# Optimization experiments

Measured on AMD Instinct MI355X. Metric: run time of the kernel, lower is better.

The kernel has to match this reference:

```python
import jax, jax.numpy as jnp
import numpy as np
import math

H = 12  # num_heads
LOGIT_SCALE_MAX = math.log(1.0 / 0.01)  # ~4.60517


def setup_inputs() -> dict:
    key = jax.random.key(0)
    ks = jax.random.split(key, 4)
    L, N, C = 1024, 8, 768
    scale = (C // H) ** -0.5
    return {
        "x": jax.random.normal(ks[0], (L, N, C), jnp.float32),
        "in_proj_weight": jax.random.normal(ks[1], (3 * C, C), jnp.float32) * scale,
        "in_proj_bias": jnp.zeros((3 * C,), jnp.float32),
        "logit_scale": jnp.full((H, 1, 1), jnp.log(10.0), jnp.float32),
        "head_scale": jnp.ones((H, 1, 1), jnp.float32),
        "out_w": jax.random.normal(ks[2], (C, C), jnp.float32) * scale,
        "out_b": jnp.zeros((C,), jnp.float32),
    }


def _normalize(t, eps=1e-12):
    # torch F.normalize: x / max(||x||, eps)
    n = jnp.linalg.norm(t, axis=-1, keepdims=True)
    return t / jnp.maximum(n, eps)


def reference(x, in_proj_weight, in_proj_bias, logit_scale, head_scale, out_w, out_b):
    L, N, C = x.shape
    D = C // H
    qkv = x @ in_proj_weight.T + in_proj_bias  # (L, N, 3C)
    q, k, v = jnp.split(qkv, 3, axis=-1)

    def to_heads(t):  # (L, N, C) -> (N, H, L, D); matches view(L, N*H, D).transpose(0,1)
        return t.reshape(L, N, H, D).transpose(1, 2, 0, 3)

    q, k, v = to_heads(q), to_heads(k), to_heads(v)
    # scaled-cosine attention: cosine sim * clamped-exp learnable logit scale
    attn = jnp.einsum('nhld,nhmd->nhlm', _normalize(q), _normalize(k))  # (N,H,L,L)
    ls = jnp.exp(jnp.minimum(logit_scale, LOGIT_SCALE_MAX))  # (H,1,1)
    attn = attn * ls[None]
    attn = jax.nn.softmax(attn, axis=-1)
    o = jnp.einsum('nhlm,nhmd->nhld', attn, v)  # (N,H,L,D)
    o = o * head_scale[None]  # per-head scale
    o = o.transpose(2, 0, 1, 3).reshape(L, N, C)  # back to (L, N, C)
    return o @ out_w.T + out_b
```

## Files before the change

### kernel.cpp

```cpp
#include <hip/hip_runtime.h>
#include <stdint.h>
#include <math.h>

typedef unsigned short u16;
typedef _Float16 f16;
typedef __attribute__((ext_vector_type(4))) float f32x4;
typedef __attribute__((ext_vector_type(8))) f16 h8;
typedef __attribute__((ext_vector_type(4))) f16 h4;
typedef __attribute__((ext_vector_type(2))) f16 h2;
typedef __attribute__((ext_vector_type(2))) __fp16 fp16x2;
typedef __attribute__((ext_vector_type(2))) unsigned int u32x2;
typedef __attribute__((ext_vector_type(4))) unsigned int u32x4;
typedef __attribute__((ext_vector_type(4))) unsigned short u16x4;
typedef __attribute__((ext_vector_type(8))) unsigned short u16x8;

typedef const __attribute__((address_space(1))) u16 gas_u16;
typedef __attribute__((address_space(3))) u16 las_u16;

#define MFMA32(a,b,c) __builtin_amdgcn_mfma_f32_16x16x32_f16((a),(b),(c),0,0,0)
#define MFMA16(a,b,c) __builtin_amdgcn_mfma_f32_16x16x16f16((a),(b),(c),0,0,0)

__device__ __forceinline__ float h2f(u16 h){ f16 x; __builtin_memcpy(&x,&h,2); return (float)x; }
__device__ __forceinline__ u16 f2h(float f){ f16 x = (f16)f; u16 u; __builtin_memcpy(&u,&x,2); return u; }

__device__ __forceinline__ float fast_exp2(float x){
#if __has_builtin(__builtin_amdgcn_exp2f)
  return __builtin_amdgcn_exp2f(x);
#else
  return exp2f(x);
#endif
}

__device__ __forceinline__ h2 pkrtz(float a, float b){
  fp16x2 t = __builtin_amdgcn_cvt_pkrtz(a, b);
  h2 r; __builtin_memcpy(&r, &t, 4);
  return r;
}

#define NA4 1572864
#define NB4 442368
#define NC4 147456
__global__ __launch_bounds__(256) void cvt3_kernel(
    const float* __restrict__ a, u16* __restrict__ da,
    const float* __restrict__ b, u16* __restrict__ db,
    const float* __restrict__ c, u16* __restrict__ dc)
{
  int i = blockIdx.x*256 + threadIdx.x;
  const float* s; u16* d; int off;
  if (i < NA4)            { s = a; d = da; off = i; }
  else if (i < NA4+NB4)   { s = b; d = db; off = i - NA4; }
  else if (i < NA4+NB4+NC4){ s = c; d = dc; off = i - NA4 - NB4; }
  else return;
  f32x4 v = ((const f32x4*)s)[off];
  u16x4 o;
  o[0]=f2h(v[0]); o[1]=f2h(v[1]); o[2]=f2h(v[2]); o[3]=f2h(v[3]);
  ((u16x4*)d)[off] = o;
}

__global__ __launch_bounds__(256) void gemm_kernel(
    const u16* __restrict__ A, const u16* __restrict__ B, const float* __restrict__ bias,
    int mode, u16* __restrict__ qh, u16* __restrict__ kh, u16* __restrict__ vtp,
    float* __restrict__ outp, const float* __restrict__ lsb)
{
  __shared__ u16 lA[2][128*64];
  __shared__ u16 lB[2][128*64];
  const int tid = threadIdx.x;
  const int lane = tid & 63;
  const int w = tid >> 6, wr = w >> 1, wc = w & 1;
  const int lo = lane & 15, hi = lane >> 4;

  const int bx = blockIdx.x, by = blockIdx.y;

  f32x4 zero = {0.f,0.f,0.f,0.f};
  f32x4 acc[4][4];
#pragma unroll
  for (int a=0;a<4;a++)
#pragma unroll
    for (int b=0;b<4;b++) acc[a][b] = zero;
  const u16* Ag = A + (size_t)bx*128*768;
  const u16* Bg = B + (size_t)by*128*768;
  const int srow = tid >> 3;
  const int scol = (((tid & 7) ^ (srow & 7)) * 8);

#define STAGE(buf, kt) do { \
    _Pragma("unroll") \
    for (int j=0;j<4;j++) { \
      __builtin_amdgcn_global_load_lds((gas_u16*)(Ag + (size_t)(j*32+srow)*768 + (kt) + scol), (las_u16*)(&lA[buf][j*2048 + tid*8]), 16, 0, 0); \
      __builtin_amdgcn_global_load_lds((gas_u16*)(Bg + (size_t)(j*32+srow)*768 + (kt) + scol), (las_u16*)(&lB[buf][j*2048 + tid*8]), 16, 0, 0); \
    } \
  } while(0)

  STAGE(0, 0);
#pragma unroll
  for (int t = 0; t < 12; ++t) {
    const int cur = t & 1;
    if (t < 11) {
      STAGE(cur^1, (t+1)*64);
      asm volatile("s_waitcnt vmcnt(8)" ::: "memory");
    } else {
      asm volatile("s_waitcnt vmcnt(0)" ::: "memory");
    }
    __builtin_amdgcn_sched_barrier(0);
    __builtin_amdgcn_s_barrier();
#pragma unroll
    for (int s=0;s<2;s++) {
      const int kk = s ^ (w & 1);
      h8 af[4], bfr[4];
#pragma unroll
      for (int mf=0; mf<4; mf++) {
        int r = wr*64 + mf*16 + lo;
        af[mf]  = *(const h8*)(&lA[cur][r*64 + (((hi + 4*kk) ^ (lo & 7)) * 8)]);
      }
#pragma unroll
      for (int nf=0; nf<4; nf++) {
        int r = wc*64 + nf*16 + lo;
        bfr[nf] = *(const h8*)(&lB[cur][r*64 + (((hi + 4*kk) ^ (lo & 7)) * 8)]);
      }
#pragma unroll
      for (int mf=0; mf<4; mf++)
#pragma unroll
        for (int nf=0; nf<4; nf++)
          acc[mf][nf] = MFMA32(af[mf], bfr[nf], acc[mf][nf]);
    }
    asm volatile("s_waitcnt lgkmcnt(0)" ::: "memory");
    __builtin_amdgcn_sched_barrier(0);
    __builtin_amdgcn_s_barrier();
  }
#undef STAGE

  const int r0 = bx*128 + wr*64;
  const int j0 = by*128 + wc*64;
  if (mode == 0) {
    const int p = (j0 >= 1536) ? 2 : ((j0 >= 768) ? 1 : 0);
    float bi[4];
#pragma unroll
    for (int nf=0;nf<4;nf++) bi[nf] = bias[j0 + nf*16 + lo];
    if (p == 2) {
      u16* Tt = (wc == 0) ? (u16*)lA : (u16*)lB;
      const int cbase = wr*16;
#pragma unroll
      for (int mf=0; mf<4; mf++)
#pragma unroll
        for (int nf=0; nf<4; nf++) {
          int d = nf*16 + lo;
          int c = cbase + mf*4 + hi;
          u16x4 pk;
#pragma unroll
          for (int i=0;i<4;i++) pk[i] = f2h(acc[mf][nf][i] + bi[nf]);
          *(u16x4*)(Tt + d*128 + ((c ^ ((d & 7) << 2)) << 2)) = pk;
        }
      __syncthreads();
      const int hh0 = 2*by - 24;
#pragma unroll
      for (int kq=0; kq<8; kq++) {
        int idx = tid + kq*256;
        int nn  = idx & 7;
        int d   = (idx >> 3) & 63;
        int lh  = (idx >> 9) & 1;
        int wcc = idx >> 10;
        const u16* Ts = (wcc == 0) ? (const u16*)lA : (const u16*)lB;
        u16x8 v8;
#pragma unroll
        for (int ll=0; ll<8; ll++) {
          int rl = (lh*8 + ll)*8 + nn;
          int c  = rl >> 2;
          v8[ll] = Ts[d*128 + ((c ^ ((d & 7) << 2)) << 2) + (rl & 3)];
        }
        size_t off = (((size_t)nn*12 + hh0 + wcc)*64 + d)*1024 + (size_t)bx*16 + lh*8;
        *(u16x8*)(vtp + off) = v8;
      }
    } else {
      const int c0 = j0 - p*768;
      const int hh = c0 >> 6;
      u16* dst = (p==0) ? qh : kh;
      float qsc = 1.0f;
      if (p == 0) qsc = __expf(fminf(lsb[hh], 4.6051701859880913680f)) * 1.4426950408889634f;
#pragma unroll
      for (int mf=0; mf<4; mf++)
#pragma unroll
        for (int i=0;i<4;i++) {
          int r = r0 + mf*16 + 4*hi + i;
          int n = r & 7, l = r >> 3;
          float v[4]; float ss = 0.f;
#pragma unroll
          for (int nf=0;nf<4;nf++){ v[nf] = acc[mf][nf][i] + bi[nf]; ss += v[nf]*v[nf]; }
          ss += __shfl_xor(ss, 1);
          ss += __shfl_xor(ss, 2);
          ss += __shfl_xor(ss, 4);
          ss += __shfl_xor(ss, 8);
          float sc = qsc / fmaxf(sqrtf(ss), 1e-12f);
          size_t base = (((size_t)n*12 + hh)*1024 + l)*64;
#pragma unroll
          for (int nf=0;nf<4;nf++)
            dst[base + nf*16 + lo] = f2h(v[nf]*sc);
        }
    }
  } else {
#pragma unroll
    for (int nf=0; nf<4; nf++) {
      int j = j0 + nf*16 + lo;
      float bi = bias[j];
#pragma unroll
      for (int mf=0; mf<4; mf++)
#pragma unroll
        for (int i=0;i<4;i++) {
          int r = r0 + mf*16 + 4*hi + i;
          outp[(size_t)r*768 + j] = acc[mf][nf][i] + bi;
        }
    }
  }
}

__global__ __launch_bounds__(256, 3) void flash_kernel(
    const u16* __restrict__ qh, const u16* __restrict__ kh, const u16* __restrict__ vt,
    u16* __restrict__ obuf, const float* __restrict__ hsv, const float* __restrict__ lsp)
{
  __shared__ u16 lK[2][64*64];
  __shared__ u16 lVT[2][64*64];
  const int lin = blockIdx.y*8 + blockIdx.x;
  const int xcd = lin & 7, g = lin >> 3;
  const int nh = xcd + 8*(g >> 3);
  const int qt = g & 7;
  const int h = nh % 12, n = nh / 12;
  const u16* Qp = qh + (size_t)nh*65536;
  const u16* Kp = kh + (size_t)nh*65536;
  const u16* Vp = vt + (size_t)nh*65536;
  const int tid = threadIdx.x, lane = tid & 63, w = tid >> 6;
  const int lo = lane & 15, hi = lane >> 4;
  const int e = lo & 7;

  h8 qa0, qa1, qb0, qb1;
  {
    const u16* qrow = Qp + (size_t)(qt*128 + w*32 + lo)*64 + hi*8;
    qa0 = *(const h8*)qrow;          qa1 = *(const h8*)(qrow + 32);
    qb0 = *(const h8*)(qrow + 1024); qb1 = *(const h8*)(qrow + 1024 + 32);
  }
  const f32x4 zero = {0.f,0.f,0.f,0.f};
  f32x4 oA[4] = {zero,zero,zero,zero};
  f32x4 oB[4] = {zero,zero,zero,zero};
  f32x4 lA4 = zero, lB4 = zero;
  const h4 ones = {(f16)1.f,(f16)1.f,(f16)1.f,(f16)1.f};

  float OFF;
  {
    float b = __expf(fminf(lsp[h], 4.6051701859880913680f)) * 1.4426950408889634f;
    OFF = fmaxf(b - 15.5f, 0.f);
  }

  const int sr = tid >> 2;
  const int c4 = tid & 3;
  const int sx1 = sr & 7;
  const int sx2 = (sr & 7) << 1;

  u32x4 ka, kb, va, vb;
  ka = *(const u32x4*)(Kp + (size_t)sr*64 + c4*16);
  kb = *(const u32x4*)(Kp + (size_t)sr*64 + c4*16 + 8);
  va = *(const u32x4*)(Vp + (size_t)sr*1024 + c4*16);
  vb = *(const u32x4*)(Vp + (size_t)sr*1024 + c4*16 + 8);

#define STAGE_WRITE(bf) do { \
    u16* kr = lK[bf] + sr*64; \
    *(u32x4*)(kr + (((2*c4)   ^ sx1) << 3)) = ka; \
    *(u32x4*)(kr + (((2*c4+1) ^ sx1) << 3)) = kb; \
    u16* vr = lVT[bf] + sr*64; \
    *(u32x2*)(vr + (((( 0|c4) ^ sx2) << 2))) = (u32x2){va[0], va[1]}; \
    *(u32x2*)(vr + (((( 4|c4) ^ sx2) << 2))) = (u32x2){va[2], va[3]}; \
    *(u32x2*)(vr + (((( 8|c4) ^ sx2) << 2))) = (u32x2){vb[0], vb[1]}; \
    *(u32x2*)(vr + ((((12|c4) ^ sx2) << 2))) = (u32x2){vb[2], vb[3]}; \
  } while(0)

  STAGE_WRITE(0);
  asm volatile("s_waitcnt lgkmcnt(0)" ::: "memory");
  __builtin_amdgcn_sched_barrier(0);
  __builtin_amdgcn_s_barrier();

  for (int t = 0; t < 16; ++t) {
    const int cb = t & 1;
    if (t < 15) {
      ka = *(const u32x4*)(Kp + (size_t)(t+1)*4096 + (size_t)sr*64 + c4*16);
      kb = *(const u32x4*)(Kp + (size_t)(t+1)*4096 + (size_t)sr*64 + c4*16 + 8);
      va = *(const u32x4*)(Vp + (size_t)sr*1024 + (t+1)*64 + c4*16);
      vb = *(const u32x4*)(Vp + (size_t)sr*1024 + (t+1)*64 + c4*16 + 8);
    }
    f32x4 sa[4], sb[4];
#pragma unroll
    for (int kf=0; kf<4; kf++) {
      const u16* krow = lK[cb] + (kf*16 + lo)*64;
      h8 k0 = *(const h8*)(krow + (((hi  ) ^ e) << 3));
      h8 k1 = *(const h8*)(krow + (((hi+4) ^ e) << 3));
      sa[kf] = MFMA32(k1, qa1, MFMA32(k0, qa0, zero));
      sb[kf] = MFMA32(k1, qb1, MFMA32(k0, qb0, zero));
    }
    if (OFF != 0.f) {
#pragma unroll
      for (int kf=0;kf<4;kf++)
#pragma unroll
        for (int i=0;i<4;i++) { sa[kf][i] -= OFF; sb[kf][i] -= OFF; }
    }
    h4 pa[4], pb[4];
#pragma unroll
    for (int kf=0;kf<4;kf++) {
      h2 a01 = pkrtz(fast_exp2(sa[kf][0]), fast_exp2(sa[kf][1]));
      h2 a23 = pkrtz(fast_exp2(sa[kf][2]), fast_exp2(sa[kf][3]));
      pa[kf] = __builtin_shufflevector(a01, a23, 0, 1, 2, 3);
      h2 b01 = pkrtz(fast_exp2(sb[kf][0]), fast_exp2(sb[kf][1]));
      h2 b23 = pkrtz(fast_exp2(sb[kf][2]), fast_exp2(sb[kf][3]));
      pb[kf] = __builtin_shufflevector(b01, b23, 0, 1, 2, 3);
    }
#pragma unroll
    for (int kf=0;kf<4;kf++) {
      lA4 = MFMA16(ones, pa[kf], lA4);
      lB4 = MFMA16(ones, pb[kf], lB4);
    }
#pragma unroll
    for (int db=0; db<4; db++) {
      const u16* vrow = lVT[cb] + (db*16 + lo)*64;
      h8 v01 = *(const h8*)(vrow + ((((2*hi  ) ^ e) << 3)));
      h8 v23 = *(const h8*)(vrow + ((((2*hi+1) ^ e) << 3)));
      h4 f0 = __builtin_shufflevector(v01, v01, 0,1,2,3);
      h4 f1 = __builtin_shufflevector(v01, v01, 4,5,6,7);
      h4 f2 = __builtin_shufflevector(v23, v23, 0,1,2,3);
      h4 f3 = __builtin_shufflevector(v23, v23, 4,5,6,7);
      oA[db] = MFMA16(f0, pa[0], oA[db]);
      oB[db] = MFMA16(f0, pb[0], oB[db]);
      oA[db] = MFMA16(f1, pa[1], oA[db]);
      oB[db] = MFMA16(f1, pb[1], oB[db]);
      oA[db] = MFMA16(f2, pa[2], oA[db]);
      oB[db] = MFMA16(f2, pb[2], oB[db]);
      oA[db] = MFMA16(f3, pa[3], oA[db]);
      oB[db] = MFMA16(f3, pb[3], oB[db]);
    }
    if (t < 15) STAGE_WRITE(cb ^ 1);
    asm volatile("s_waitcnt lgkmcnt(0)" ::: "memory");
    __builtin_amdgcn_sched_barrier(0);
    __builtin_amdgcn_s_barrier();
  }
#undef STAGE_WRITE
  float hsc = hsv[h];
  float invA = hsc / lA4[0];
  float invB = hsc / lB4[0];
  int l0 = qt*128 + w*32 + lo;
  u16* dA = obuf + ((size_t)l0*8 + n)*768 + h*64;
  u16* dB = obuf + ((size_t)(l0+16)*8 + n)*768 + h*64;
#pragma unroll
  for (int db=0; db<4; db++) {
    u16x4 pk0, pk1;
#pragma unroll
    for (int i=0;i<4;i++) { pk0[i] = f2h(oA[db][i]*invA); pk1[i] = f2h(oB[db][i]*invB); }
    *(u16x4*)(dA + db*16 + hi*4) = pk0;
    *(u16x4*)(dB + db*16 + hi*4) = pk1;
  }
}

extern "C" void kernel_launch(void* const* d_in, const int* in_sizes, int n_in,
                              void* d_out, int out_size, void* d_ws, size_t ws_size,
                              hipStream_t stream)
{
  (void)in_sizes; (void)n_in; (void)out_size; (void)ws_size;
  const float* x  = (const float*)d_in[0];
  const float* w1 = (const float*)d_in[1];
  const float* b1 = (const float*)d_in[2];
  const float* ls = (const float*)d_in[3];
  const float* hs = (const float*)d_in[4];
  const float* w2 = (const float*)d_in[5];
  const float* b2 = (const float*)d_in[6];
  float* out = (float*)d_out;

  u16* x_bf  = (u16*)d_ws;
  u16* w1_bf = x_bf  + 6291456;
  u16* w2_bf = w1_bf + 1769472;
  u16* qh    = w2_bf + 589824;
  u16* kh    = qh    + 6291456;
  u16* vt    = kh    + 6291456;
  u16* ob    = x_bf;

  cvt3_kernel<<<8448, 256, 0, stream>>>(x, x_bf, w1, w1_bf, w2, w2_bf);
  gemm_kernel<<<dim3(64,18), 256, 0, stream>>>(x_bf, w1_bf, b1, 0, qh, kh, vt, nullptr, ls);
  flash_kernel<<<dim3(8,96), 256, 0, stream>>>(qh, kh, vt, ob, hs, ls);
  gemm_kernel<<<dim3(64,6), 256, 0, stream>>>(ob, w2_bf, b2, 1, nullptr, nullptr, nullptr, out, ls);
}
```

Measured before the change: 117.4 us.

## Enlarge GEMM tile to 128x256 with 512 threads and triple-buffered LDS pipeline

The projection GEMM moves from 128x128 tiles with 4 waves to 128x256 tiles with 8 waves. The K loop becomes a three-slot LDS ring that prefetches two steps ahead, splits each stage's loads across the two k sub-steps, and raises wave priority around the MFMA blocks. The goal is to halve A-tile reloads and hide global-to-LDS latency behind compute. The cost is fewer blocks (576 and 192), which may underfill the GPU's CUs, plus about 144KB of LDS per block, which limits occupancy.

```diff
diff --git a/kernel.cpp b/kernel.cpp
--- a/kernel.cpp
+++ b/kernel.cpp
@@ -57,16 +57,17 @@
   ((u16x4*)d)[off] = o;
 }
 
-__global__ __launch_bounds__(256) void gemm_kernel(
+#define GSLOT 24576
+__global__ __launch_bounds__(512, 2) void gemm_kernel(
     const u16* __restrict__ A, const u16* __restrict__ B, const float* __restrict__ bias,
     int mode, u16* __restrict__ qh, u16* __restrict__ kh, u16* __restrict__ vtp,
     float* __restrict__ outp, const float* __restrict__ lsb)
 {
-  __shared__ u16 lA[2][128*64];
-  __shared__ u16 lB[2][128*64];
+  __shared__ u16 L[3*GSLOT];
   const int tid = threadIdx.x;
   const int lane = tid & 63;
-  const int w = tid >> 6, wr = w >> 1, wc = w & 1;
+  const int w = tid >> 6;
+  const int wm = w >> 2, wn = w & 3;
   const int lo = lane & 15, hi = lane >> 4;
 
   const int bx = blockIdx.x, by = blockIdx.y;
@@ -78,87 +79,93 @@
 #pragma unroll
     for (int b=0;b<4;b++) acc[a][b] = zero;
   const u16* Ag = A + (size_t)bx*128*768;
-  const u16* Bg = B + (size_t)by*128*768;
+  const u16* Bg = B + (size_t)by*256*768;
   const int srow = tid >> 3;
   const int scol = (((tid & 7) ^ (srow & 7)) * 8);
 
-#define STAGE(buf, kt) do { \
-    _Pragma("unroll") \
-    for (int j=0;j<4;j++) { \
-      __builtin_amdgcn_global_load_lds((gas_u16*)(Ag + (size_t)(j*32+srow)*768 + (kt) + scol), (las_u16*)(&lA[buf][j*2048 + tid*8]), 16, 0, 0); \
-      __builtin_amdgcn_global_load_lds((gas_u16*)(Bg + (size_t)(j*32+srow)*768 + (kt) + scol), (las_u16*)(&lB[buf][j*2048 + tid*8]), 16, 0, 0); \
+#define STG(slot, kt, half) do { \
+    if ((half) == 0) { \
+      __builtin_amdgcn_global_load_lds((gas_u16*)(Ag + (size_t)srow*768 + (kt) + scol),      (las_u16*)(&L[(slot)*GSLOT + tid*8]),        16, 0, 0); \
+      __builtin_amdgcn_global_load_lds((gas_u16*)(Ag + (size_t)(srow+64)*768 + (kt) + scol), (las_u16*)(&L[(slot)*GSLOT + 4096 + tid*8]), 16, 0, 0); \
+      __builtin_amdgcn_global_load_lds((gas_u16*)(Bg + (size_t)srow*768 + (kt) + scol),      (las_u16*)(&L[(slot)*GSLOT + 8192 + tid*8]), 16, 0, 0); \
+    } else { \
+      __builtin_amdgcn_global_load_lds((gas_u16*)(Bg + (size_t)(srow+64)*768 + (kt) + scol),  (las_u16*)(&L[(slot)*GSLOT + 12288 + tid*8]), 16, 0, 0); \
+      __builtin_amdgcn_global_load_lds((gas_u16*)(Bg + (size_t)(srow+128)*768 + (kt) + scol), (las_u16*)(&L[(slot)*GSLOT + 16384 + tid*8]), 16, 0, 0); \
+      __builtin_amdgcn_global_load_lds((gas_u16*)(Bg + (size_t)(srow+192)*768 + (kt) + scol), (las_u16*)(&L[(slot)*GSLOT + 20480 + tid*8]), 16, 0, 0); \
     } \
   } while(0)
 
-  STAGE(0, 0);
-#pragma unroll
+  STG(0, 0, 0);  STG(0, 0, 1);
+  STG(1, 64, 0); STG(1, 64, 1);
+  asm volatile("s_waitcnt vmcnt(6)" ::: "memory");
+  __builtin_amdgcn_sched_barrier(0);
+  __builtin_amdgcn_s_barrier();
+
+  int cs = 0;
   for (int t = 0; t < 12; ++t) {
-    const int cur = t & 1;
-    if (t < 11) {
-      STAGE(cur^1, (t+1)*64);
-      asm volatile("s_waitcnt vmcnt(8)" ::: "memory");
-    } else {
-      asm volatile("s_waitcnt vmcnt(0)" ::: "memory");
-    }
-    __builtin_amdgcn_sched_barrier(0);
-    __builtin_amdgcn_s_barrier();
-#pragma unroll
-    for (int s=0;s<2;s++) {
-      const int kk = s ^ (w & 1);
+    const u16* LA = L + cs*GSLOT;
+    const u16* LB = LA + 8192;
+    int ss = cs + 2; if (ss >= 3) ss -= 3;
+#pragma unroll
+    for (int kk = 0; kk < 2; ++kk) {
+      const int rsl = ((hi + 4*kk) ^ (lo & 7)) * 8;
       h8 af[4], bfr[4];
 #pragma unroll
-      for (int mf=0; mf<4; mf++) {
-        int r = wr*64 + mf*16 + lo;
-        af[mf]  = *(const h8*)(&lA[cur][r*64 + (((hi + 4*kk) ^ (lo & 7)) * 8)]);
-      }
-#pragma unroll
-      for (int nf=0; nf<4; nf++) {
-        int r = wc*64 + nf*16 + lo;
-        bfr[nf] = *(const h8*)(&lB[cur][r*64 + (((hi + 4*kk) ^ (lo & 7)) * 8)]);
-      }
+      for (int mf=0; mf<4; mf++) af[mf]  = *(const h8*)(LA + (wm*64 + mf*16 + lo)*64 + rsl);
+#pragma unroll
+      for (int nf=0; nf<4; nf++) bfr[nf] = *(const h8*)(LB + (wn*64 + nf*16 + lo)*64 + rsl);
+      if (t < 10) STG(ss, (t+2)*64, kk);
+      __builtin_amdgcn_s_barrier();
+      asm volatile("s_waitcnt lgkmcnt(0)" ::: "memory");
+      __builtin_amdgcn_sched_barrier(0);
+      __builtin_amdgcn_s_setprio(1);
 #pragma unroll
       for (int mf=0; mf<4; mf++)
 #pragma unroll
         for (int nf=0; nf<4; nf++)
           acc[mf][nf] = MFMA32(af[mf], bfr[nf], acc[mf][nf]);
-    }
-    asm volatile("s_waitcnt lgkmcnt(0)" ::: "memory");
-    __builtin_amdgcn_sched_barrier(0);
-    __builtin_amdgcn_s_barrier();
-  }
-#undef STAGE
-
-  const int r0 = bx*128 + wr*64;
-  const int j0 = by*128 + wc*64;
+      __builtin_amdgcn_s_setprio(0);
+      if (kk == 1) {
+        if (t < 10)       asm volatile("s_waitcnt vmcnt(6)" ::: "memory");
+        else if (t == 10) asm volatile("s_waitcnt vmcnt(0)" ::: "memory");
+        __builtin_amdgcn_sched_barrier(0);
+      }
+      __builtin_amdgcn_s_barrier();
+    }
+    cs += 1; if (cs >= 3) cs -= 3;
+  }
+#undef STG
+
+  const int r0 = bx*128 + wm*64;
+  const int j0 = by*256 + wn*64;
   if (mode == 0) {
     const int p = (j0 >= 1536) ? 2 : ((j0 >= 768) ? 1 : 0);
     float bi[4];
 #pragma unroll
     for (int nf=0;nf<4;nf++) bi[nf] = bias[j0 + nf*16 + lo];
     if (p == 2) {
-      u16* Tt = (wc == 0) ? (u16*)lA : (u16*)lB;
-      const int cbase = wr*16;
+      u16* Tt = (u16*)L + wn*8192;
 #pragma unroll
       for (int mf=0; mf<4; mf++)
 #pragma unroll
         for (int nf=0; nf<4; nf++) {
           int d = nf*16 + lo;
-          int c = cbase + mf*4 + hi;
+          int c = wm*16 + mf*4 + hi;
           u16x4 pk;
 #pragma unroll
           for (int i=0;i<4;i++) pk[i] = f2h(acc[mf][nf][i] + bi[nf]);
           *(u16x4*)(Tt + d*128 + ((c ^ ((d & 7) << 2)) << 2)) = pk;
         }
       __syncthreads();
-      const int hh0 = 2*by - 24;
 #pragma unroll
       for (int kq=0; kq<8; kq++) {
-        int idx = tid + kq*256;
+        int idx = tid + kq*512;
         int nn  = idx & 7;
         int d   = (idx >> 3) & 63;
         int lh  = (idx >> 9) & 1;
-        int wcc = idx >> 10;
-        const u16* Ts = (wcc == 0) ? (const u16*)lA : (const u16*)lB;
+        int tw  = idx >> 10;
+        const u16* Ts = (const u16*)L + tw*8192;
+        int hh = (by - 6)*4 + tw;
         u16x8 v8;
 #pragma unroll
         for (int ll=0; ll<8; ll++) {
@@ -166,7 +173,7 @@
           int c  = rl >> 2;
           v8[ll] = Ts[d*128 + ((c ^ ((d & 7) << 2)) << 2) + (rl & 3)];
         }
-        size_t off = (((size_t)nn*12 + hh0 + wcc)*64 + d)*1024 + (size_t)bx*16 + lh*8;
+        size_t off = (((size_t)nn*12 + hh)*64 + d)*1024 + (size_t)bx*16 + lh*8;
         *(u16x8*)(vtp + off) = v8;
       }
     } else {
@@ -181,14 +188,14 @@
         for (int i=0;i<4;i++) {
           int r = r0 + mf*16 + 4*hi + i;
           int n = r & 7, l = r >> 3;
-          float v[4]; float ss = 0.f;
-#pragma unroll
-          for (int nf=0;nf<4;nf++){ v[nf] = acc[mf][nf][i] + bi[nf]; ss += v[nf]*v[nf]; }
-          ss += __shfl_xor(ss, 1);
-          ss += __shfl_xor(ss, 2);
-          ss += __shfl_xor(ss, 4);
-          ss += __shfl_xor(ss, 8);
-          float sc = qsc / fmaxf(sqrtf(ss), 1e-12f);
+          float v[4]; float ss2 = 0.f;
+#pragma unroll
+          for (int nf=0;nf<4;nf++){ v[nf] = acc[mf][nf][i] + bi[nf]; ss2 += v[nf]*v[nf]; }
+          ss2 += __shfl_xor(ss2, 1);
+          ss2 += __shfl_xor(ss2, 2);
+          ss2 += __shfl_xor(ss2, 4);
+          ss2 += __shfl_xor(ss2, 8);
+          float sc = qsc / fmaxf(sqrtf(ss2), 1e-12f);
           size_t base = (((size_t)n*12 + hh)*1024 + l)*64;
 #pragma unroll
           for (int nf=0;nf<4;nf++)
@@ -375,7 +382,7 @@
   u16* ob    = x_bf;
 
   cvt3_kernel<<<8448, 256, 0, stream>>>(x, x_bf, w1, w1_bf, w2, w2_bf);
-  gemm_kernel<<<dim3(64,18), 256, 0, stream>>>(x_bf, w1_bf, b1, 0, qh, kh, vt, nullptr, ls);
+  gemm_kernel<<<dim3(64,9), 512, 0, stream>>>(x_bf, w1_bf, b1, 0, qh, kh, vt, nullptr, ls);
   flash_kernel<<<dim3(8,96), 256, 0, stream>>>(qh, kh, vt, ob, hs, ls);
-  gemm_kernel<<<dim3(64,6), 256, 0, stream>>>(ob, w2_bf, b2, 1, nullptr, nullptr, nullptr, out, ls);
-}
+  gemm_kernel<<<dim3(64,3), 512, 0, stream>>>(ob, w2_bf, b2, 1, nullptr, nullptr, nullptr, out, ls);
+}
```

Result: faster. 114.4 us (median of 2 runs) (-2.6%).
